# Optimization experiments

Measured on AMD Instinct MI355X. Metric: run time of the kernel, lower is better.

Reference implementation:

```python
import jax, jax.numpy as jnp
import numpy as np

N_NODES = 100000
N_EDGES = 3200000
N_FEAT = 64
N_CLASS = 16


def setup_inputs() -> dict:
    key = jax.random.key(0)
    k1, k2, k3, k4 = jax.random.split(key, 4)
    x = jax.random.normal(k1, (N_NODES, N_FEAT), dtype=jnp.float32)
    weight = jax.random.normal(k2, (N_CLASS, N_FEAT), dtype=jnp.float32) * 0.1
    bias = jax.random.normal(k3, (N_CLASS,), dtype=jnp.float32) * 0.1
    edge_index = jax.random.randint(k4, (2, N_EDGES), 0, N_NODES, dtype=jnp.int64)
    return {"x": x, "weight": weight, "bias": bias, "edge_index": edge_index, "k": 3}


def reference(x, weight, bias, edge_index, k):
    # SGConv: x' = (D^-1/2 (A + I) D^-1/2)^K X, then Linear, then log_softmax.
    n = x.shape[0]
    loop = jnp.arange(n, dtype=edge_index.dtype)
    src = jnp.concatenate([edge_index[0], loop])  # add self-loops
    dst = jnp.concatenate([edge_index[1], loop])
    # gcn_norm: degree over destination nodes (edge weights all ones)
    deg = jax.ops.segment_sum(jnp.ones_like(src, dtype=x.dtype), dst, num_segments=n)
    dis = jnp.where(deg > 0, jax.lax.rsqrt(jnp.maximum(deg, 1)), 0.0).astype(x.dtype)
    norm = dis[src] * dis[dst]  # [E + N]
    for _ in range(k):
        # gather source features, scale, scatter-add to destinations
        x = jax.ops.segment_sum(x[src] * norm[:, None], dst, num_segments=n)
    logits = x @ weight.T + bias  # [N, C]
    return jax.nn.log_softmax(logits, axis=1)
```

## Files before the change

kernel.cpp:

```cpp
#include <hip/hip_runtime.h>
#include <hip/hip_fp16.h>

#define NFEAT 64
#define NCLS 16
#define MAXDEG 96
#define BSH 7
#define BSIZE 128
#define NBLK 512
#define NBMAX 1024
#define EPB 6272
#define CAP 4480
#define MINCP 48

__global__ void k_hist(const int* __restrict__ dst, int* __restrict__ G,
                       int nE, int epb, int nb) {
    __shared__ int h[NBMAX];
    int j = blockIdx.x;
    for (int t = threadIdx.x; t < nb; t += blockDim.x) h[t] = 0;
    __syncthreads();
    int e0 = j * epb, e1 = min(e0 + epb, nE);
    for (int e = e0 + threadIdx.x; e < e1; e += blockDim.x)
        atomicAdd(&h[dst[e] >> BSH], 1);
    __syncthreads();
    for (int t = threadIdx.x; t < nb; t += blockDim.x)
        G[(size_t)j * nb + t] = h[t];
}

__global__ void k_gscan(const int* __restrict__ G, int* __restrict__ btot,
                        int* __restrict__ BASE, int nb) {
    __shared__ int wt[NBLK / 64];
    int b = blockIdx.x, t = threadIdx.x;
    int lane = t & 63, wv = t >> 6;
    int v = G[(size_t)t * nb + b];
    int s = v;
#pragma unroll
    for (int off = 1; off < 64; off <<= 1) {
        int u = __shfl_up(s, off);
        if (lane >= off) s += u;
    }
    if (lane == 63) wt[wv] = s;
    __syncthreads();
    int pre = 0, tot = 0;
#pragma unroll
    for (int w = 0; w < NBLK / 64; ++w) {
        if (w < wv) pre += wt[w];
        tot += wt[w];
    }
    if (t == 0) btot[b] = tot;
    BASE[(size_t)t * nb + b] = b * CAP + pre + s - v;
}

__global__ void k_binsort(const int* __restrict__ src, const int* __restrict__ dst,
                          const int* __restrict__ G, const int* __restrict__ BASE,
                          int* __restrict__ pairs, int nE, int epb, int nb) {
    __shared__ int ebuf[EPB];
    __shared__ int gbuf[EPB];
    __shared__ int loc[NBMAX];
    __shared__ int gb[NBMAX];
    __shared__ int wt[NBMAX / 64];
    int j = blockIdx.x, tid = threadIdx.x;
    int lane = tid & 63, wv = tid >> 6;
    int v = (tid < nb) ? G[(size_t)j * nb + tid] : 0;
    int s = v;
#pragma unroll
    for (int off = 1; off < 64; off <<= 1) {
        int u = __shfl_up(s, off);
        if (lane >= off) s += u;
    }
    if (lane == 63) wt[wv] = s;
    __syncthreads();
    int pre = 0;
#pragma unroll
    for (int w = 0; w < NBMAX / 64; ++w) if (w < wv) pre += wt[w];
    int excl = pre + s - v;
    loc[tid] = excl;
    if (tid < nb) gb[tid] = BASE[(size_t)j * nb + tid] - excl;
    __syncthreads();
    int e0 = j * epb, e1 = min(e0 + epb, nE);
    for (int e = e0 + tid; e < e1; e += blockDim.x) {
        int d = dst[e], ssrc = src[e];
        int b = d >> BSH;
        int p = atomicAdd(&loc[b], 1);
        ebuf[p] = ((d & (BSIZE - 1)) << 17) | ssrc;
        gbuf[p] = gb[b] + p;
    }
    __syncthreads();
    int m = e1 - e0;
    for (int p = tid; p < m; p += blockDim.x)
        pairs[gbuf[p]] = ebuf[p];
}

__global__ void k_csr(const int* __restrict__ pairs, const int* __restrict__ btot,
                      int* __restrict__ ssortP, int4* __restrict__ aux,
                      float* __restrict__ dis, int n, int nb) {
    __shared__ int buf[BSIZE][MAXDEG];
    __shared__ int cnt[BSIZE];
    int b = blockIdx.x;
    for (int t = threadIdx.x; t < BSIZE; t += blockDim.x) cnt[t] = 0;
    __syncthreads();
    int e0 = b * CAP, e1 = e0 + btot[b];
    for (int e = e0 + threadIdx.x; e < e1; e += blockDim.x) {
        int pk = pairs[e];
        int s = pk & 0x1FFFF;
        int ld = ((unsigned)pk) >> 17;
        int p = atomicAdd(&cnt[ld], 1);
        if (p < MAXDEG) buf[ld][p] = s;
    }
    __syncthreads();
    for (int idx = threadIdx.x; idx < BSIZE * MAXDEG; idx += blockDim.x) {
        int ld = idx / MAXDEG, p = idx - ld * MAXDEG;
        int node = (b << BSH) + ld;
        int c = min(cnt[ld], MAXDEG - 1);
        int cp = (c + 1 + 15) & ~15;
        if (cp < MINCP) cp = MINCP;
        if (node < n && p < cp) {
            int val = (p < c) ? buf[ld][p] : ((p == c) ? node : n);
            ssortP[(size_t)node * MAXDEG + p] = val;
        }
    }
    int node = (b << BSH) + threadIdx.x;
    if (threadIdx.x < BSIZE && node < n) {
        int c = min(cnt[threadIdx.x], MAXDEG - 1);
        float d = (float)(c + 1);
        float ds = rsqrtf(d);
        dis[node] = ds;
        aux[node] = make_int4(c + 1, __float_as_int(ds * ds), __float_as_int(sqrtf(d)), 0);
    }
}

__global__ void k_lin0(const float* __restrict__ x, const float* __restrict__ w,
                       const float* __restrict__ dis, __half* __restrict__ za,
                       __half* __restrict__ zb, int n) {
    __shared__ float4 ws4[NCLS * 17];
    for (int i = threadIdx.x; i < NCLS * 16; i += blockDim.x) {
        int c = i >> 4, j = i & 15;
        ws4[c * 17 + j] = ((const float4*)w)[i];
    }
    __syncthreads();
    int t = blockIdx.x * blockDim.x + threadIdx.x;
    int node = t >> 2;
    if (node > n) return;
    int q = t & 3;
    if (node == n) {
        ((int2*)(za + (size_t)n * NCLS))[q] = make_int2(0, 0);
        ((int2*)(zb + (size_t)n * NCLS))[q] = make_int2(0, 0);
        return;
    }
    const float4* xr = (const float4*)(x + (size_t)node * NFEAT);
    const float4* wq = &ws4[(q << 2) * 17];
    float a0 = 0.f, a1 = 0.f, a2 = 0.f, a3 = 0.f;
#pragma unroll
    for (int j = 0; j < 16; ++j) {
        float4 v  = xr[j];
        float4 w0 = wq[j];
        float4 w1 = wq[17 + j];
        float4 w2 = wq[34 + j];
        float4 w3 = wq[51 + j];
        a0 += v.x * w0.x + v.y * w0.y + v.z * w0.z + v.w * w0.w;
        a1 += v.x * w1.x + v.y * w1.y + v.z * w1.z + v.w * w1.w;
        a2 += v.x * w2.x + v.y * w2.y + v.z * w2.z + v.w * w2.w;
        a3 += v.x * w3.x + v.y * w3.y + v.z * w3.z + v.w * w3.w;
    }
    float d = dis[node];
    __half2 h01 = __floats2half2_rn(a0 * d, a1 * d);
    __half2 h23 = __floats2half2_rn(a2 * d, a3 * d);
    __half2* o = (__half2*)(za + (size_t)node * NCLS) + (q << 1);
    o[0] = h01;
    o[1] = h23;
}

__device__ inline void acc8(int4 v, float* a) {
    __half2 t; float2 f;
    *(int*)&t = v.x; f = __half22float2(t); a[0] += f.x; a[1] += f.y;
    *(int*)&t = v.y; f = __half22float2(t); a[2] += f.x; a[3] += f.y;
    *(int*)&t = v.z; f = __half22float2(t); a[4] += f.x; a[5] += f.y;
    *(int*)&t = v.w; f = __half22float2(t); a[6] += f.x; a[7] += f.y;
}
__device__ inline int pkh2(float x, float y) {
    __half2 r = __floats2half2_rn(x, y);
    return *(int*)&r;
}

template <bool FINAL>
__global__ void __launch_bounds__(256, 8)
k_prop16(const __half* __restrict__ zin, __half* __restrict__ zout,
         const int4* __restrict__ aux, const int* __restrict__ ssortP,
         const float* __restrict__ bias, float* __restrict__ out, int n) {
    int t = blockIdx.x * blockDim.x + threadIdx.x;
    int wid = t >> 6;
    int lane = threadIdx.x & 63;
    int g2 = lane >> 4;
    int e3 = (lane >> 1) & 7;
    int h8 = (lane & 1) << 3;
    int node = wid * 4 + g2;
    bool valid = node < n;
    int nd = valid ? node : (n - 1);
    const int* row = ssortP + (size_t)nd * MAXDEG + 2 * e3;
    int2 r0 = *(const int2*)(row);
    int2 r1 = *(const int2*)(row + 16);
    int2 r2 = *(const int2*)(row + 32);
    int4 ax = aux[nd];
    int dg = ax.x;
    if (dg > MAXDEG) dg = MAXDEG;
    int2 r3 = make_int2(n, n), r4 = r3, r5 = r3;
    if (dg > 48) r3 = *(const int2*)(row + 48);
    if (dg > 64) r4 = *(const int2*)(row + 64);
    if (dg > 80) r5 = *(const int2*)(row + 80);
    float a[8] = {0.f, 0.f, 0.f, 0.f, 0.f, 0.f, 0.f, 0.f};
#define GATH2(rr) { \
        int4 vA = *(const int4*)(zin + (size_t)(rr).x * NCLS + h8); \
        int4 vB = *(const int4*)(zin + (size_t)(rr).y * NCLS + h8); \
        acc8(vA, a); acc8(vB, a); }
    GATH2(r0);
    GATH2(r1);
    GATH2(r2);
    if (dg > 48) GATH2(r3);
    if (dg > 64) GATH2(r4);
    if (dg > 80) GATH2(r5);
#undef GATH2
#pragma unroll
    for (int i = 0; i < 8; ++i) {
        a[i] += __shfl_xor(a[i], 2);
        a[i] += __shfl_xor(a[i], 4);
        a[i] += __shfl_xor(a[i], 8);
    }
    float d2 = __int_as_float(ax.y);
    if (!FINAL) {
        if (valid && e3 == 0) {
            int4 o = make_int4(pkh2(a[0] * d2, a[1] * d2), pkh2(a[2] * d2, a[3] * d2),
                               pkh2(a[4] * d2, a[5] * d2), pkh2(a[6] * d2, a[7] * d2));
            *(int4*)(zout + (size_t)node * NCLS + h8) = o;
        }
    } else {
        float rd = __int_as_float(ax.z);
        float sc = d2 * rd;
        int hq = h8 >> 2;
        float4 b0 = ((const float4*)bias)[hq];
        float4 b1 = ((const float4*)bias)[hq + 1];
        float lg[8];
        lg[0] = a[0] * sc + b0.x; lg[1] = a[1] * sc + b0.y;
        lg[2] = a[2] * sc + b0.z; lg[3] = a[3] * sc + b0.w;
        lg[4] = a[4] * sc + b1.x; lg[5] = a[5] * sc + b1.y;
        lg[6] = a[6] * sc + b1.z; lg[7] = a[7] * sc + b1.w;
        float m = fmaxf(fmaxf(fmaxf(lg[0], lg[1]), fmaxf(lg[2], lg[3])),
                        fmaxf(fmaxf(lg[4], lg[5]), fmaxf(lg[6], lg[7])));
        m = fmaxf(m, __shfl_xor(m, 1));
        float s = 0.f;
#pragma unroll
        for (int i = 0; i < 8; ++i) s += expf(lg[i] - m);
        s += __shfl_xor(s, 1);
        float lse = m + logf(s);
        if (valid && e3 == 0) {
            float* orow = out + (size_t)node * NCLS + h8;
            ((float4*)orow)[0] = make_float4(lg[0] - lse, lg[1] - lse, lg[2] - lse, lg[3] - lse);
            ((float4*)orow)[1] = make_float4(lg[4] - lse, lg[5] - lse, lg[6] - lse, lg[7] - lse);
        }
    }
}

extern "C" void kernel_launch(void* const* d_in, const int* in_sizes, int n_in,
                              void* d_out, int out_size, void* d_ws, size_t ws_size,
                              hipStream_t stream) {
    const float* x    = (const float*)d_in[0];
    const float* w    = (const float*)d_in[1];
    const float* bias = (const float*)d_in[2];
    const int*   ei   = (const int*)d_in[3];

    int n  = in_sizes[0] / NFEAT;
    int nE = in_sizes[3] / 2;
    const int* src = ei;
    const int* dst = ei + nE;

    int nb  = (n + BSIZE - 1) >> BSH;
    int epb = (nE + NBLK - 1) / NBLK;

    char* p = (char*)d_ws;
    auto alloc = [&](size_t bytes) { void* r = (void*)p; p += (bytes + 511) & ~511ULL; return r; };
    int*    ssortP = (int*)alloc((size_t)n * MAXDEG * 4);
    int*    pairs  = (int*)alloc((size_t)nb * CAP * 4);
    __half* za     = (__half*)alloc((size_t)(n + 1) * NCLS * 2);
    __half* zb     = (__half*)alloc((size_t)(n + 1) * NCLS * 2);
    int*    G      = (int*)alloc((size_t)NBLK * nb * 4);
    int*    BASE   = (int*)alloc((size_t)NBLK * nb * 4);
    int*    btot   = (int*)alloc((size_t)nb * 4);
    int4*   aux    = (int4*)G;
    float*  dis    = (float*)BASE;

    k_hist   <<<NBLK, 1024, 0, stream>>>(dst, G, nE, epb, nb);
    k_gscan  <<<nb, NBLK, 0, stream>>>(G, btot, BASE, nb);
    k_binsort<<<NBLK, 1024, 0, stream>>>(src, dst, G, BASE, pairs, nE, epb, nb);
    k_csr    <<<nb, 512, 0, stream>>>(pairs, btot, ssortP, aux, dis, n, nb);

    k_lin0<<<(4 * (n + 1) + 255) / 256, 256, 0, stream>>>(x, w, dis, za, zb, n);

    int nblk = (int)((((size_t)(n + 3) / 4) * 64 + 255) / 256);
    k_prop16<false><<<nblk, 256, 0, stream>>>(za, zb, aux, ssortP, bias, nullptr, n);
    k_prop16<false><<<nblk, 256, 0, stream>>>(zb, za, aux, ssortP, bias, nullptr, n);
    k_prop16<true> <<<nblk, 256, 0, stream>>>(za, nullptr, aux, ssortP, bias, (float*)d_out, n);
}
```

Measured before the change: 120.7 us.

## Fuse histogram and scan into binsort with global atomic bucket offsets

Removes the separate histogram and global scan kernels. Each binsort block now builds its local histogram itself and claims space in every bucket with a global atomicAdd on a per-bucket counter, so two launches and the G/BASE round-trips go away. This makes edge order inside a bucket nondeterministic, which can change floating-point summation order. Separately, the propagation kernel now loads and gathers the third neighbor chunk only when degree exceeds 32, skipping that work for low-degree nodes.

Result: slower. 132.0 us (+9.4%).

```diff
diff --git a/kernel.cpp b/kernel.cpp
--- a/kernel.cpp
+++ b/kernel.cpp
@@ -10,57 +10,25 @@
 #define NBMAX 1024
 #define EPB 6272
 #define CAP 4480
-#define MINCP 48
-
-__global__ void k_hist(const int* __restrict__ dst, int* __restrict__ G,
-                       int nE, int epb, int nb) {
-    __shared__ int h[NBMAX];
-    int j = blockIdx.x;
-    for (int t = threadIdx.x; t < nb; t += blockDim.x) h[t] = 0;
-    __syncthreads();
-    int e0 = j * epb, e1 = min(e0 + epb, nE);
-    for (int e = e0 + threadIdx.x; e < e1; e += blockDim.x)
-        atomicAdd(&h[dst[e] >> BSH], 1);
-    __syncthreads();
-    for (int t = threadIdx.x; t < nb; t += blockDim.x)
-        G[(size_t)j * nb + t] = h[t];
-}
-
-__global__ void k_gscan(const int* __restrict__ G, int* __restrict__ btot,
-                        int* __restrict__ BASE, int nb) {
-    __shared__ int wt[NBLK / 64];
-    int b = blockIdx.x, t = threadIdx.x;
-    int lane = t & 63, wv = t >> 6;
-    int v = G[(size_t)t * nb + b];
-    int s = v;
-#pragma unroll
-    for (int off = 1; off < 64; off <<= 1) {
-        int u = __shfl_up(s, off);
-        if (lane >= off) s += u;
-    }
-    if (lane == 63) wt[wv] = s;
-    __syncthreads();
-    int pre = 0, tot = 0;
-#pragma unroll
-    for (int w = 0; w < NBLK / 64; ++w) {
-        if (w < wv) pre += wt[w];
-        tot += wt[w];
-    }
-    if (t == 0) btot[b] = tot;
-    BASE[(size_t)t * nb + b] = b * CAP + pre + s - v;
-}
+#define MINCP 32
 
 __global__ void k_binsort(const int* __restrict__ src, const int* __restrict__ dst,
-                          const int* __restrict__ G, const int* __restrict__ BASE,
-                          int* __restrict__ pairs, int nE, int epb, int nb) {
+                          int* __restrict__ gcnt, int* __restrict__ pairs,
+                          int nE, int epb, int nb) {
     __shared__ int ebuf[EPB];
     __shared__ int gbuf[EPB];
-    __shared__ int loc[NBMAX];
+    __shared__ int cnt[NBMAX];
     __shared__ int gb[NBMAX];
     __shared__ int wt[NBMAX / 64];
     int j = blockIdx.x, tid = threadIdx.x;
     int lane = tid & 63, wv = tid >> 6;
-    int v = (tid < nb) ? G[(size_t)j * nb + tid] : 0;
+    cnt[tid] = 0;
+    __syncthreads();
+    int e0 = j * epb, e1 = min(e0 + epb, nE);
+    for (int e = e0 + tid; e < e1; e += blockDim.x)
+        atomicAdd(&cnt[dst[e] >> BSH], 1);
+    __syncthreads();
+    int v = cnt[tid];
     int s = v;
 #pragma unroll
     for (int off = 1; off < 64; off <<= 1) {
@@ -73,14 +41,17 @@
 #pragma unroll
     for (int w = 0; w < NBMAX / 64; ++w) if (w < wv) pre += wt[w];
     int excl = pre + s - v;
-    loc[tid] = excl;
-    if (tid < nb) gb[tid] = BASE[(size_t)j * nb + tid] - excl;
-    __syncthreads();
-    int e0 = j * epb, e1 = min(e0 + epb, nE);
+    cnt[tid] = excl;
+    if (tid < nb) {
+        int g = tid * CAP;
+        if (v > 0) g += atomicAdd(&gcnt[tid], v);
+        gb[tid] = g - excl;
+    }
+    __syncthreads();
     for (int e = e0 + tid; e < e1; e += blockDim.x) {
         int d = dst[e], ssrc = src[e];
         int b = d >> BSH;
-        int p = atomicAdd(&loc[b], 1);
+        int p = atomicAdd(&cnt[b], 1);
         ebuf[p] = ((d & (BSIZE - 1)) << 17) | ssrc;
         gbuf[p] = gb[b] + p;
     }
@@ -195,14 +166,14 @@
     int node = wid * 4 + g2;
     bool valid = node < n;
     int nd = valid ? node : (n - 1);
+    int4 ax = aux[nd];
     const int* row = ssortP + (size_t)nd * MAXDEG + 2 * e3;
     int2 r0 = *(const int2*)(row);
     int2 r1 = *(const int2*)(row + 16);
-    int2 r2 = *(const int2*)(row + 32);
-    int4 ax = aux[nd];
     int dg = ax.x;
     if (dg > MAXDEG) dg = MAXDEG;
-    int2 r3 = make_int2(n, n), r4 = r3, r5 = r3;
+    int2 r2 = make_int2(n, n), r3 = r2, r4 = r2, r5 = r2;
+    if (dg > 32) r2 = *(const int2*)(row + 32);
     if (dg > 48) r3 = *(const int2*)(row + 48);
     if (dg > 64) r4 = *(const int2*)(row + 64);
     if (dg > 80) r5 = *(const int2*)(row + 80);
@@ -213,7 +184,7 @@
         acc8(vA, a); acc8(vB, a); }
     GATH2(r0);
     GATH2(r1);
-    GATH2(r2);
+    if (dg > 32) GATH2(r2);
     if (dg > 48) GATH2(r3);
     if (dg > 64) GATH2(r4);
     if (dg > 80) GATH2(r5);
@@ -280,16 +251,13 @@
     int*    pairs  = (int*)alloc((size_t)nb * CAP * 4);
     __half* za     = (__half*)alloc((size_t)(n + 1) * NCLS * 2);
     __half* zb     = (__half*)alloc((size_t)(n + 1) * NCLS * 2);
-    int*    G      = (int*)alloc((size_t)NBLK * nb * 4);
-    int*    BASE   = (int*)alloc((size_t)NBLK * nb * 4);
-    int*    btot   = (int*)alloc((size_t)nb * 4);
-    int4*   aux    = (int4*)G;
-    float*  dis    = (float*)BASE;
-
-    k_hist   <<<NBLK, 1024, 0, stream>>>(dst, G, nE, epb, nb);
-    k_gscan  <<<nb, NBLK, 0, stream>>>(G, btot, BASE, nb);
-    k_binsort<<<NBLK, 1024, 0, stream>>>(src, dst, G, BASE, pairs, nE, epb, nb);
-    k_csr    <<<nb, 512, 0, stream>>>(pairs, btot, ssortP, aux, dis, n, nb);
+    int4*   aux    = (int4*)alloc((size_t)n * 16);
+    float*  dis    = (float*)alloc((size_t)n * 4);
+    int*    gcnt   = (int*)alloc((size_t)nb * 4);
+
+    hipMemsetAsync(gcnt, 0, (size_t)nb * 4, stream);
+    k_binsort<<<NBLK, 1024, 0, stream>>>(src, dst, gcnt, pairs, nE, epb, nb);
+    k_csr    <<<nb, 512, 0, stream>>>(pairs, gcnt, ssortP, aux, dis, n, nb);
 
     k_lin0<<<(4 * (n + 1) + 255) / 256, 256, 0, stream>>>(x, w, dis, za, zb, n);
 
```
